# Optimization experiments

Hardware: AMD Instinct MI355X
Metric: run time of the kernel (lower is better)

Reference implementation:

```python
import jax, jax.numpy as jnp
import numpy as np

B, C, N = 16, 3, 4096
K = 20
IN_CH, HID, OUT_CH = 2 * C, 64, 64
EPS = 1e-5
NEG_SLOPE = 0.2


def setup_inputs() -> dict:
    key = jax.random.key(0)
    ks = jax.random.split(key, 4)
    return {
        "x": jax.random.normal(ks[0], (B, C, N), dtype=jnp.float32),
        "W1": jax.random.normal(ks[1], (HID, IN_CH), dtype=jnp.float32) * 0.1,
        "W2": jax.random.normal(ks[2], (HID, HID), dtype=jnp.float32) * 0.1,
        "W3": jax.random.normal(ks[3], (OUT_CH, HID), dtype=jnp.float32) * 0.1,
        "g1": jnp.ones((HID,), jnp.float32),
        "b1": jnp.zeros((HID,), jnp.float32),
        "g2": jnp.ones((OUT_CH,), jnp.float32),
        "b2": jnp.zeros((OUT_CH,), jnp.float32),
    }


def _lrelu(y):
    return jnp.where(y > 0, y, NEG_SLOPE * y)


def _bn(y, gamma, beta):
    # training-mode BatchNorm2d: stats over all axes except channel (last here)
    mu = jnp.mean(y, axis=(0, 1, 2), keepdims=True)
    var = jnp.mean((y - mu) ** 2, axis=(0, 1, 2), keepdims=True)
    return (y - mu) * jax.lax.rsqrt(var + EPS) * gamma + beta


def _graph_feature(x, k):
    # x: [B, C, N] -> DGCNN edge features [B, N, k, 2C]
    xt = jnp.transpose(x, (0, 2, 1))  # [B, N, C]
    sq = jnp.sum(xt * xt, axis=-1)    # [B, N]
    # negative squared pairwise distance (top_k picks nearest, incl. self)
    neg_dist = 2.0 * jnp.einsum('bnc,bmc->bnm', xt, xt) - sq[:, :, None] - sq[:, None, :]
    _, idx = jax.lax.top_k(neg_dist, k)                 # [B, N, k]
    nbr = jax.vmap(lambda xb, ib: xb[ib])(xt, idx)      # [B, N, k, C] gather
    xc = jnp.broadcast_to(xt[:, :, None, :], nbr.shape)
    return jnp.concatenate([nbr - xc, xc], axis=-1)     # [B, N, k, 2C]


def reference(x, W1, W2, W3, g1, b1, g2, b2):
    f = _graph_feature(x, K)                    # [B, N, k, 2C]
    # 1x1 convs over channel axis (last), matching NCHW permute(0,3,2,1)
    y = jnp.einsum('bnkc,oc->bnko', f, W1)
    y = _bn(_lrelu(y), g1, b1)
    y = jnp.einsum('bnkc,oc->bnko', y, W2)
    y = _bn(_lrelu(y), g1, b1)                  # norm1 is reused (shared params)
    y = jnp.einsum('bnkc,oc->bnko', y, W3)
    y = _bn(_lrelu(y), g2, b2)
    y = jnp.max(y, axis=2)                      # max over k neighbors -> [B, N, out]
    return jnp.transpose(y, (0, 2, 1))          # [B, out, N]
```

## Files before the change

### kernel.cpp

```cpp
#include <hip/hip_runtime.h>
#include <math.h>

#define KNN 20
#define CNT_INV (1.0f / 1310720.0f)

typedef short bf16x8 __attribute__((ext_vector_type(8)));
typedef float f32x4  __attribute__((ext_vector_type(4)));

__device__ __forceinline__ short f2bf(float f) {
  unsigned u = __builtin_bit_cast(unsigned, f);
  u += 0x7FFFu + ((u >> 16) & 1u);
  return (short)(u >> 16);
}
__device__ __forceinline__ float lrelu(float y) { return y > 0.f ? y : 0.2f * y; }

__global__ __launch_bounds__(256) void xt4_kernel(const float* __restrict__ x,
                                                  float4* __restrict__ xt4) {
  const int t = blockIdx.x * 256 + threadIdx.x;
  const int b = t >> 12, m = t & 4095;
  const float* xb = x + (size_t)b * 12288;
  const float a = xb[m], c = xb[4096 + m], e = xb[8192 + m];
  xt4[t] = make_float4(a, c, e, a * a + c * c + e * e);
}

__global__ __launch_bounds__(256) void knn_kernel(const float4* __restrict__ xt4,
                                                  int* __restrict__ idx_out,
                                                  const float* __restrict__ W1,
                                                  float* __restrict__ s1buf) {
  __shared__ int hist[512];
  __shared__ int sB[4];
  __shared__ int wcnt[2][4];
  __shared__ int slist[2][64];
  __shared__ int scnt[2];
  __shared__ int eidx[2][KNN];
  __shared__ float redS[2][128], redQ[2][128];
  const int tid = threadIdx.x, lane = tid & 63, wid = tid >> 6;
  const int p0 = blockIdx.x * 2;
  const int b = p0 >> 12, n0 = p0 & 4095;
  const float4* xb4 = xt4 + (size_t)b * 4096;
  const float4 cpa = xb4[n0], cpb = xb4[n0 + 1];

  float w1r[6];
#pragma unroll
  for (int c = 0; c < 6; ++c) w1r[c] = W1[lane * 6 + c];

  float da[16], db[16];
#pragma unroll
  for (int i = 0; i < 16; ++i) {
    const float4 qv = xb4[i * 256 + tid];
    const float dta = fmaf(cpa.x, qv.x, fmaf(cpa.y, qv.y, cpa.z * qv.z));
    const float dtb = fmaf(cpb.x, qv.x, fmaf(cpb.y, qv.y, cpb.z * qv.z));
    da[i] = fmaxf(fmaf(-2.0f, dta, qv.w) + cpa.w, 0.0f);
    db[i] = fmaxf(fmaf(-2.0f, dtb, qv.w) + cpb.w, 0.0f);
  }

  float lo0 = 0.f, R0 = 1.f, lo1 = 0.f, R1 = 1.f;
  int before0 = 0, before1 = 0;
  float Dedge0 = 1e30f, Dedge1 = 1e30f;
  bool done0 = false, done1 = false;
  for (int pass = 0; pass < 6 && !(done0 && done1); ++pass) {
    hist[tid] = 0; hist[256 + tid] = 0;
    __syncthreads();
    const float sc0 = 256.0f / R0, sc1 = 256.0f / R1;
#pragma unroll
    for (int i = 0; i < 16; ++i) {
      if (!done0) {
        const float rel = da[i] - lo0;
        if (rel >= 0.0f && rel < R0) {
          int bin = (int)(rel * sc0); bin = bin > 255 ? 255 : bin;
          atomicAdd(&hist[bin], 1);
        }
      }
      if (!done1) {
        const float rel = db[i] - lo1;
        if (rel >= 0.0f && rel < R1) {
          int bin = (int)(rel * sc1); bin = bin > 255 ? 255 : bin;
          atomicAdd(&hist[256 + bin], 1);
        }
      }
    }
    __syncthreads();
    if (wid < 2) {
      const bool skip = wid ? done1 : done0;
      if (!skip) {
        const int* h = &hist[wid * 256];
        int s0 = h[lane], s1 = h[64 + lane], s2 = h[128 + lane], s3 = h[192 + lane];
#pragma unroll
        for (int off = 1; off < 64; off <<= 1) { const int t = __shfl_up(s0, off); if (lane >= off) s0 += t; }
#pragma unroll
        for (int off = 1; off < 64; off <<= 1) { const int t = __shfl_up(s1, off); if (lane >= off) s1 += t; }
#pragma unroll
        for (int off = 1; off < 64; off <<= 1) { const int t = __shfl_up(s2, off); if (lane >= off) s2 += t; }
#pragma unroll
        for (int off = 1; off < 64; off <<= 1) { const int t = __shfl_up(s3, off); if (lane >= off) s3 += t; }
        s1 += __shfl(s0, 63);
        s2 += __shfl(s1, 63);
        s3 += __shfl(s2, 63);
        const int bef = wid ? before1 : before0;
        s0 += bef; s1 += bef; s2 += bef; s3 += bef;
        int B = 256, cnt = 0;
        unsigned long long m = __ballot(s0 >= 20);
        if (m) { const int l = __ffsll((long long)m) - 1; B = l; cnt = __shfl(s0, l); }
        else if ((m = __ballot(s1 >= 20)) != 0ull) { const int l = __ffsll((long long)m) - 1; B = 64 + l; cnt = __shfl(s1, l); }
        else if ((m = __ballot(s2 >= 20)) != 0ull) { const int l = __ffsll((long long)m) - 1; B = 128 + l; cnt = __shfl(s2, l); }
        else if ((m = __ballot(s3 >= 20)) != 0ull) { const int l = __ffsll((long long)m) - 1; B = 192 + l; cnt = __shfl(s3, l); }
        if (lane == 0) { sB[wid * 2] = B; sB[wid * 2 + 1] = cnt; }
      }
    }
    __syncthreads();
    bool zoom0 = false, zoom1 = false;
    if (!done0) {
      const int B = sB[0], cnt = sB[1];
      if (B == 256) R0 *= 16.0f;
      else {
        const float bw = R0 * (1.0f / 256.0f);
        Dedge0 = lo0 + (float)(B + 1) * bw;
        if (cnt <= 48) done0 = true;
        else { lo0 += (float)B * bw; R0 = bw; zoom0 = true; }
      }
    }
    if (!done1) {
      const int B = sB[2], cnt = sB[3];
      if (B == 256) R1 *= 16.0f;
      else {
        const float bw = R1 * (1.0f / 256.0f);
        Dedge1 = lo1 + (float)(B + 1) * bw;
        if (cnt <= 48) done1 = true;
        else { lo1 += (float)B * bw; R1 = bw; zoom1 = true; }
      }
    }
    if (zoom0) {
      int c = 0;
#pragma unroll
      for (int i = 0; i < 16; ++i) c += (int)__popcll(__ballot(da[i] < lo0));
      if (lane == 0) wcnt[0][wid] = c;
    }
    if (zoom1) {
      int c = 0;
#pragma unroll
      for (int i = 0; i < 16; ++i) c += (int)__popcll(__ballot(db[i] < lo1));
      if (lane == 0) wcnt[1][wid] = c;
    }
    if (zoom0 || zoom1) {
      __syncthreads();
      if (zoom0) before0 = wcnt[0][0] + wcnt[0][1] + wcnt[0][2] + wcnt[0][3];
      if (zoom1) before1 = wcnt[1][0] + wcnt[1][1] + wcnt[1][2] + wcnt[1][3];
    }
  }

  if (tid < 2) scnt[tid] = 0;
  __syncthreads();
  const float Dthr0 = Dedge0 + 4e-3f, Dthr1 = Dedge1 + 4e-3f;
#pragma unroll
  for (int i = 0; i < 16; ++i) {
    if (da[i] < Dthr0) {
      const int pos = atomicAdd(&scnt[0], 1);
      if (pos < 64) slist[0][pos] = i * 256 + tid;
    }
    if (db[i] < Dthr1) {
      const int pos = atomicAdd(&scnt[1], 1);
      if (pos < 64) slist[1][pos] = i * 256 + tid;
    }
  }
  __syncthreads();

  if (wid < 2) {
    const int s = min(scnt[wid], 64);
    const float4 cp = wid ? cpb : cpa;
    int myi = -1; double myd = -1.0e300;
    if (lane < s) {
      myi = slist[wid][lane];
      const float4 av = xb4[myi];
      const double c0 = (double)cp.x, c1 = (double)cp.y, c2 = (double)cp.z;
      const double a0 = (double)av.x, a1 = (double)av.y, a2 = (double)av.z;
      const double dot = c0 * a0 + c1 * a1 + c2 * a2;
      const double sqm = a0 * a0 + a1 * a1 + a2 * a2;
      const double sn  = c0 * c0 + c1 * c1 + c2 * c2;
      myd = (2.0 * dot - sn) - sqm;
    }
    int rank = 0;
    for (int j = 0; j < s; ++j) {
      const double od = __shfl(myd, j);
      const int    oi = __shfl(myi, j);
      if (od > myd || (od == myd && oi < myi)) ++rank;
    }
    if (lane < s && rank < KNN) {
      idx_out[(p0 + wid) * KNN + rank] = myi;
      eidx[wid][rank] = myi;
    }
  }
  __syncthreads();

  const int q = wid >> 1, kb = wid & 1;
  const float4 cp = q ? cpb : cpa;
  float sm = 0.f, sq = 0.f;
#pragma unroll
  for (int t = 0; t < 10; ++t) {
    const int kk = eidx[q][kb * 10 + t];
    const float4 qv = xb4[kk];
    float y = w1r[0] * (qv.x - cp.x) + w1r[1] * (qv.y - cp.y) +
              w1r[2] * (qv.z - cp.z) +
              w1r[3] * cp.x + w1r[4] * cp.y + w1r[5] * cp.z;
    y = lrelu(y);
    sm += y; sq += y * y;
  }
  redS[q][kb * 64 + lane] = sm; redQ[q][kb * 64 + lane] = sq;
  __syncthreads();
  if (tid < 128) {
    const int q2 = tid >> 6, l2 = tid & 63;
    const float s  = redS[q2][l2] + redS[q2][64 + l2];
    const float qq = redQ[q2][l2] + redQ[q2][64 + l2];
    float* bk = s1buf + (size_t)((p0 + q2) & 255) * 128;
    atomicAdd(&bk[l2], s);
    atomicAdd(&bk[64 + l2], qq);
  }
}

template <int STAGE, int MINW>
__global__ __launch_bounds__(256, MINW) void stage_kernel(
    const float4* __restrict__ xt4, const int* __restrict__ nbr,
    const float* __restrict__ W1,
    const float* __restrict__ w2ft, const float* __restrict__ b2f,
    const float* __restrict__ w3ft, const float* __restrict__ b3f,
    float* __restrict__ sumO, float* __restrict__ sqO,
    float* __restrict__ mx, float* __restrict__ mn) {
  __shared__ float pts[4][96];
  __shared__ float W1T[384];
  __shared__ short abuf[4][2048];
  __shared__ float redS[256], redQ[256];

  const int tid = threadIdx.x, wave = tid >> 6, lane = tid & 63;
  const int q = lane >> 4, cc = lane & 15;

  for (int i = tid; i < 384; i += 256) W1T[i] = W1[(i & 63) * 6 + (i >> 6)];
  __syncthreads();

  float w1r[6];
#pragma unroll
  for (int c = 0; c < 6; ++c) w1r[c] = W1T[c * 64 + lane];

  bf16x8 w2f[2][4];
#pragma unroll
  for (int kt = 0; kt < 2; ++kt)
#pragma unroll
    for (int nt = 0; nt < 4; ++nt)
#pragma unroll
      for (int j = 0; j < 8; ++j)
        w2f[kt][nt][j] = f2bf(w2ft[(kt * 32 + q * 8 + j) * 64 + nt * 16 + cc]);
  float bias2v[4];
#pragma unroll
  for (int nt = 0; nt < 4; ++nt) bias2v[nt] = b2f[nt * 16 + cc];

  bf16x8 w3f[2][4];
  float bias3v[4];
  if (STAGE == 3) {
#pragma unroll
    for (int kt = 0; kt < 2; ++kt)
#pragma unroll
      for (int nt = 0; nt < 4; ++nt)
#pragma unroll
        for (int j = 0; j < 8; ++j)
          w3f[kt][nt][j] = f2bf(w3ft[(kt * 32 + q * 8 + j) * 64 + nt * 16 + cc]);
#pragma unroll
    for (int nt = 0; nt < 4; ++nt) bias3v[nt] = b3f[nt * 16 + cc];
  }

  const int kt1 = lane >> 5, q1 = (lane & 31) >> 3, j1 = lane & 7;
  short* ab = abuf[wave];
  const bf16x8* ab8 = (const bf16x8*)ab;
  float* pw = pts[wave];

  float s_s[4] = {0.f, 0.f, 0.f, 0.f}, s_q[4] = {0.f, 0.f, 0.f, 0.f};
  const int wgid = blockIdx.x * 4 + wave;

  for (int it = 0; it < 8; ++it) {
    const int p = wgid + it * 8192;
    const int b = p >> 12, n = p & 4095;
    const float4* xb4 = xt4 + (size_t)b * 4096;
    if (lane < KNN) {
      const int kk = nbr[p * KNN + lane];
      *(float4*)&pw[lane * 4] = xb4[kk];
    } else if (lane == KNN) {
      *(float4*)&pw[80] = xb4[n];
    }
    const float cx0 = pw[80], cx1 = pw[81], cx2 = pw[82];

#pragma unroll
    for (int k = 0; k < KNN; ++k) {
      const float4 pk = *(const float4*)&pw[k * 4];
      const float f0 = pk.x - cx0, f1 = pk.y - cx1, f2 = pk.z - cx2;
      float y = w1r[0] * f0 + w1r[1] * f1 + w1r[2] * f2 +
                w1r[3] * cx0 + w1r[4] * cx1 + w1r[5] * cx2;
      y = lrelu(y);
      ab[(((k >> 4) * 2 + kt1) * 64 + q1 * 16 + (k & 15)) * 8 + j1] = f2bf(y);
    }

    f32x4 acc2[2][4];
#pragma unroll
    for (int mt = 0; mt < 2; ++mt)
#pragma unroll
      for (int nt = 0; nt < 4; ++nt)
        acc2[mt][nt] = f32x4{bias2v[nt], bias2v[nt], bias2v[nt], bias2v[nt]};
#pragma unroll
    for (int kt = 0; kt < 2; ++kt) {
      const bf16x8 a0 = ab8[(0 * 2 + kt) * 64 + lane];
      const bf16x8 a1 = ab8[(1 * 2 + kt) * 64 + lane];
#pragma unroll
      for (int nt = 0; nt < 4; ++nt) {
        acc2[0][nt] = __builtin_amdgcn_mfma_f32_16x16x32_bf16(a0, w2f[kt][nt], acc2[0][nt], 0, 0, 0);
        acc2[1][nt] = __builtin_amdgcn_mfma_f32_16x16x32_bf16(a1, w2f[kt][nt], acc2[1][nt], 0, 0, 0);
      }
    }

    if (STAGE == 2) {
#pragma unroll
      for (int mt = 0; mt < 2; ++mt)
#pragma unroll
        for (int nt = 0; nt < 4; ++nt)
#pragma unroll
          for (int r = 0; r < 4; ++r) {
            if (mt == 1 && q != 0) continue;
            const float y = lrelu(acc2[mt][nt][r]);
            s_s[nt] += y; s_q[nt] += y * y;
          }
    } else {
#pragma unroll
      for (int mt = 0; mt < 2; ++mt)
#pragma unroll
        for (int nt = 0; nt < 4; ++nt) {
          const int kt3 = nt >> 1;
          const int q3 = (nt & 1) * 2 + (cc >> 3);
          const int j3 = cc & 7;
#pragma unroll
          for (int r = 0; r < 4; ++r) {
            if (mt == 1 && q != 0) continue;
            const float y = lrelu(acc2[mt][nt][r]);
            ab[((mt * 2 + kt3) * 64 + q3 * 16 + q * 4 + r) * 8 + j3] = f2bf(y);
          }
        }

      f32x4 acc3[2][4];
#pragma unroll
      for (int mt = 0; mt < 2; ++mt)
#pragma unroll
        for (int nt = 0; nt < 4; ++nt)
          acc3[mt][nt] = f32x4{bias3v[nt], bias3v[nt], bias3v[nt], bias3v[nt]};
#pragma unroll
      for (int kt = 0; kt < 2; ++kt) {
        const bf16x8 a0 = ab8[(0 * 2 + kt) * 64 + lane];
        const bf16x8 a1 = ab8[(1 * 2 + kt) * 64 + lane];
#pragma unroll
        for (int nt = 0; nt < 4; ++nt) {
          acc3[0][nt] = __builtin_amdgcn_mfma_f32_16x16x32_bf16(a0, w3f[kt][nt], acc3[0][nt], 0, 0, 0);
          acc3[1][nt] = __builtin_amdgcn_mfma_f32_16x16x32_bf16(a1, w3f[kt][nt], acc3[1][nt], 0, 0, 0);
        }
      }

      float vmx[4], vmn[4];
#pragma unroll
      for (int nt = 0; nt < 4; ++nt) { vmx[nt] = -INFINITY; vmn[nt] = INFINITY; }
#pragma unroll
      for (int mt = 0; mt < 2; ++mt)
#pragma unroll
        for (int nt = 0; nt < 4; ++nt)
#pragma unroll
          for (int r = 0; r < 4; ++r) {
            if (mt == 1 && q != 0) continue;
            const float y = lrelu(acc3[mt][nt][r]);
            s_s[nt] += y; s_q[nt] += y * y;
            vmx[nt] = fmaxf(vmx[nt], y); vmn[nt] = fminf(vmn[nt], y);
          }
#pragma unroll
      for (int nt = 0; nt < 4; ++nt) {
        vmx[nt] = fmaxf(vmx[nt], __shfl_xor(vmx[nt], 16));
        vmx[nt] = fmaxf(vmx[nt], __shfl_xor(vmx[nt], 32));
        vmn[nt] = fminf(vmn[nt], __shfl_xor(vmn[nt], 16));
        vmn[nt] = fminf(vmn[nt], __shfl_xor(vmn[nt], 32));
      }
      const float omx = q == 0 ? vmx[0] : q == 1 ? vmx[1] : q == 2 ? vmx[2] : vmx[3];
      const float omn = q == 0 ? vmn[0] : q == 1 ? vmn[1] : q == 2 ? vmn[2] : vmn[3];
      mx[(size_t)p * 64 + lane] = omx;
      mn[(size_t)p * 64 + lane] = omn;
    }
  }

#pragma unroll
  for (int nt = 0; nt < 4; ++nt) {
    s_s[nt] += __shfl_xor(s_s[nt], 16); s_s[nt] += __shfl_xor(s_s[nt], 32);
    s_q[nt] += __shfl_xor(s_q[nt], 16); s_q[nt] += __shfl_xor(s_q[nt], 32);
  }
  const float ms = q == 0 ? s_s[0] : q == 1 ? s_s[1] : q == 2 ? s_s[2] : s_s[3];
  const float mq = q == 0 ? s_q[0] : q == 1 ? s_q[1] : q == 2 ? s_q[2] : s_q[3];
  redS[tid] = ms; redQ[tid] = mq;
  __syncthreads();
  if (tid < 64) {
    const float s  = redS[tid] + redS[64 + tid] + redS[128 + tid] + redS[192 + tid];
    const float qq = redQ[tid] + redQ[64 + tid] + redQ[128 + tid] + redQ[192 + tid];
    atomicAdd(&sumO[tid], s);
    atomicAdd(&sqO[tid], qq);
  }
}

__global__ void fold1_kernel(const float* __restrict__ s1buf,
                             const float* __restrict__ g, const float* __restrict__ bt,
                             const float* __restrict__ W,
                             float* __restrict__ WfT, float* __restrict__ bf) {
  __shared__ float s[64], t[64];
  const int o = threadIdx.x;
  float sm = 0.f, qq = 0.f;
  for (int k = 0; k < 256; ++k) { sm += s1buf[k * 128 + o]; qq += s1buf[k * 128 + 64 + o]; }
  const float mu = sm * CNT_INV;
  const float var = qq * CNT_INV - mu * mu;
  const float sc = g[o] / sqrtf(var + 1e-5f);
  s[o] = sc; t[o] = bt[o] - mu * sc;
  __syncthreads();
  float acc = 0.f;
  for (int c = 0; c < 64; ++c) {
    const float w = W[o * 64 + c];
    WfT[c * 64 + o] = w * s[c];
    acc += w * t[c];
  }
  bf[o] = acc;
}

__global__ void fold_kernel(const float* __restrict__ sum, const float* __restrict__ sq,
                            const float* __restrict__ g, const float* __restrict__ bt,
                            const float* __restrict__ W,
                            float* __restrict__ WfT, float* __restrict__ bf) {
  __shared__ float s[64], t[64];
  const int o = threadIdx.x;
  const float mu = sum[o] * CNT_INV;
  const float var = sq[o] * CNT_INV - mu * mu;
  const float sc = g[o] / sqrtf(var + 1e-5f);
  s[o] = sc; t[o] = bt[o] - mu * sc;
  __syncthreads();
  float acc = 0.f;
  for (int c = 0; c < 64; ++c) {
    const float w = W[o * 64 + c];
    WfT[c * 64 + o] = w * s[c];
    acc += w * t[c];
  }
  bf[o] = acc;
}

__global__ void fold3_kernel(const float* __restrict__ sum, const float* __restrict__ sq,
                             const float* __restrict__ g, const float* __restrict__ bt,
                             float* __restrict__ s3, float* __restrict__ t3) {
  const int o = threadIdx.x;
  const float mu = sum[o] * CNT_INV;
  const float var = sq[o] * CNT_INV - mu * mu;
  const float sc = g[o] / sqrtf(var + 1e-5f);
  s3[o] = sc; t3[o] = bt[o] - mu * sc;
}

__global__ __launch_bounds__(256) void final_kernel(
    const float* __restrict__ mx, const float* __restrict__ mn,
    const float* __restrict__ s3, const float* __restrict__ t3,
    float* __restrict__ out) {
  __shared__ float tmx[64][65], tmn[64][65];
  __shared__ float ss[64], tt[64];
  const int tid = threadIdx.x;
  const int P = blockIdx.x * 64;
  const int b = P >> 12, nb = P & 4095;
  if (tid < 64) { ss[tid] = s3[tid]; tt[tid] = t3[tid]; }
#pragma unroll
  for (int r = 0; r < 16; ++r) {
    const int idx = r * 256 + tid;
    const int pl = idx >> 6, ch = idx & 63;
    const size_t src = ((size_t)(P + pl)) * 64 + ch;
    tmx[pl][ch] = mx[src];
    tmn[pl][ch] = mn[src];
  }
  __syncthreads();
  const int nl = tid & 63;
#pragma unroll
  for (int r = 0; r < 16; ++r) {
    const int o = (tid >> 6) + r * 4;
    const float sc = ss[o];
    const float v = sc >= 0.f ? tmx[nl][o] : tmn[nl][o];
    out[(size_t)b * 262144 + (size_t)o * 4096 + nb + nl] = sc * v + tt[o];
  }
}

extern "C" void kernel_launch(void* const* d_in, const int* in_sizes, int n_in,
                              void* d_out, int out_size, void* d_ws, size_t ws_size,
                              hipStream_t stream) {
  const float* x  = (const float*)d_in[0];
  const float* W1 = (const float*)d_in[1];
  const float* W2 = (const float*)d_in[2];
  const float* W3 = (const float*)d_in[3];
  const float* g1 = (const float*)d_in[4];
  const float* b1 = (const float*)d_in[5];
  const float* g2 = (const float*)d_in[6];
  const float* b2 = (const float*)d_in[7];
  float* out = (float*)d_out;

  char* ws = (char*)d_ws;
  float4* xt4 = (float4*)ws;
  int* idx = (int*)(ws + 1048576);
  float* F = (float*)(ws + 6291456);
  float* sum2 = F + 0,   * sq2 = F + 64;
  float* sum3 = F + 128, * sq3 = F + 192;
  float* s1buf = F + 256;
  float* W2fT = F + 33024;
  float* b2f  = F + 37120;
  float* W3fT = F + 37184;
  float* b3f  = F + 41280;
  float* s3   = F + 41344;
  float* t3   = F + 41408;
  float* mx = (float*)(ws + 6457344);
  float* mn = mx + (size_t)16 * 4096 * 64;

  hipMemsetAsync(F, 0, 33024 * sizeof(float), stream);

  xt4_kernel<<<256, 256, 0, stream>>>(x, xt4);
  knn_kernel<<<32768, 256, 0, stream>>>(xt4, idx, W1, s1buf);
  fold1_kernel<<<1, 64, 0, stream>>>(s1buf, g1, b1, W2, W2fT, b2f);
  stage_kernel<2, 3><<<2048, 256, 0, stream>>>(xt4, idx, W1, W2fT, b2f, nullptr,
                                               nullptr, sum2, sq2, nullptr, nullptr);
  fold_kernel<<<1, 64, 0, stream>>>(sum2, sq2, g1, b1, W3, W3fT, b3f);
  stage_kernel<3, 2><<<2048, 256, 0, stream>>>(xt4, idx, W1, W2fT, b2f, W3fT,
                                               b3f, sum3, sq3, mx, mn);
  fold3_kernel<<<1, 64, 0, stream>>>(sum3, sq3, g2, b2, s3, t3);
  final_kernel<<<1024, 256, 0, stream>>>(mx, mn, s3, t3, out);
}
```

Baseline: 560.6 us.

## Process four query points per kNN block and prefetch neighbor gathers in stages

The kNN kernel now handles four query points per 256-thread block instead of two. This halves the grid and reuses each loaded candidate point across four distance computations. Every wave runs its own histogram scan and rank sort, and the layer-1 statistics are summed per wave without the extra shared-memory reduction and barrier. The stage kernels software-prefetch the next iteration's neighbor indices and gathered points into registers, and fold the W1 centre term into one precomputed base. The cost is more register pressure in the kNN kernel (four 16-element distance arrays), which may lower occupancy.

```diff
diff --git a/kernel.cpp b/kernel.cpp
--- a/kernel.cpp
+++ b/kernel.cpp
@@ -27,61 +27,88 @@
                                                   int* __restrict__ idx_out,
                                                   const float* __restrict__ W1,
                                                   float* __restrict__ s1buf) {
-  __shared__ int hist[512];
-  __shared__ int sB[4];
-  __shared__ int wcnt[2][4];
-  __shared__ int slist[2][64];
-  __shared__ int scnt[2];
-  __shared__ int eidx[2][KNN];
-  __shared__ float redS[2][128], redQ[2][128];
+  __shared__ __align__(16) int hist[1024];
+  __shared__ int sB[8];
+  __shared__ int wcnt[4][4];
+  __shared__ int slist[4][64];
+  __shared__ int scnt[4];
+  __shared__ int eidx[4][KNN];
   const int tid = threadIdx.x, lane = tid & 63, wid = tid >> 6;
-  const int p0 = blockIdx.x * 2;
+  const int p0 = blockIdx.x * 4;
   const int b = p0 >> 12, n0 = p0 & 4095;
   const float4* xb4 = xt4 + (size_t)b * 4096;
-  const float4 cpa = xb4[n0], cpb = xb4[n0 + 1];
+  const float4 cp0 = xb4[n0], cp1 = xb4[n0 + 1], cp2 = xb4[n0 + 2], cp3 = xb4[n0 + 3];
 
   float w1r[6];
 #pragma unroll
   for (int c = 0; c < 6; ++c) w1r[c] = W1[lane * 6 + c];
 
-  float da[16], db[16];
+  float d0[16], d1[16], d2[16], d3[16];
 #pragma unroll
   for (int i = 0; i < 16; ++i) {
     const float4 qv = xb4[i * 256 + tid];
-    const float dta = fmaf(cpa.x, qv.x, fmaf(cpa.y, qv.y, cpa.z * qv.z));
-    const float dtb = fmaf(cpb.x, qv.x, fmaf(cpb.y, qv.y, cpb.z * qv.z));
-    da[i] = fmaxf(fmaf(-2.0f, dta, qv.w) + cpa.w, 0.0f);
-    db[i] = fmaxf(fmaf(-2.0f, dtb, qv.w) + cpb.w, 0.0f);
-  }
-
-  float lo0 = 0.f, R0 = 1.f, lo1 = 0.f, R1 = 1.f;
-  int before0 = 0, before1 = 0;
-  float Dedge0 = 1e30f, Dedge1 = 1e30f;
-  bool done0 = false, done1 = false;
-  for (int pass = 0; pass < 6 && !(done0 && done1); ++pass) {
-    hist[tid] = 0; hist[256 + tid] = 0;
+    const float t0 = fmaf(cp0.x, qv.x, fmaf(cp0.y, qv.y, cp0.z * qv.z));
+    const float t1 = fmaf(cp1.x, qv.x, fmaf(cp1.y, qv.y, cp1.z * qv.z));
+    const float t2 = fmaf(cp2.x, qv.x, fmaf(cp2.y, qv.y, cp2.z * qv.z));
+    const float t3 = fmaf(cp3.x, qv.x, fmaf(cp3.y, qv.y, cp3.z * qv.z));
+    d0[i] = fmaxf(fmaf(-2.0f, t0, qv.w) + cp0.w, 0.0f);
+    d1[i] = fmaxf(fmaf(-2.0f, t1, qv.w) + cp1.w, 0.0f);
+    d2[i] = fmaxf(fmaf(-2.0f, t2, qv.w) + cp2.w, 0.0f);
+    d3[i] = fmaxf(fmaf(-2.0f, t3, qv.w) + cp3.w, 0.0f);
+  }
+
+  float lo0 = 0.f, R0 = 1.f, lo1 = 0.f, R1 = 1.f, lo2 = 0.f, R2 = 1.f, lo3 = 0.f, R3 = 1.f;
+  int bef0 = 0, bef1 = 0, bef2 = 0, bef3 = 0;
+  float Dedge0 = 1e30f, Dedge1 = 1e30f, Dedge2 = 1e30f, Dedge3 = 1e30f;
+  bool dn0 = false, dn1 = false, dn2 = false, dn3 = false;
+  for (int pass = 0; pass < 6 && !(dn0 && dn1 && dn2 && dn3); ++pass) {
+    *(int4*)&hist[tid * 4] = int4{0, 0, 0, 0};
     __syncthreads();
     const float sc0 = 256.0f / R0, sc1 = 256.0f / R1;
-#pragma unroll
-    for (int i = 0; i < 16; ++i) {
-      if (!done0) {
-        const float rel = da[i] - lo0;
+    const float sc2 = 256.0f / R2, sc3 = 256.0f / R3;
+    if (!dn0) {
+#pragma unroll
+      for (int i = 0; i < 16; ++i) {
+        const float rel = d0[i] - lo0;
         if (rel >= 0.0f && rel < R0) {
           int bin = (int)(rel * sc0); bin = bin > 255 ? 255 : bin;
           atomicAdd(&hist[bin], 1);
         }
       }
-      if (!done1) {
-        const float rel = db[i] - lo1;
+    }
+    if (!dn1) {
+#pragma unroll
+      for (int i = 0; i < 16; ++i) {
+        const float rel = d1[i] - lo1;
         if (rel >= 0.0f && rel < R1) {
           int bin = (int)(rel * sc1); bin = bin > 255 ? 255 : bin;
           atomicAdd(&hist[256 + bin], 1);
         }
       }
     }
+    if (!dn2) {
+#pragma unroll
+      for (int i = 0; i < 16; ++i) {
+        const float rel = d2[i] - lo2;
+        if (rel >= 0.0f && rel < R2) {
+          int bin = (int)(rel * sc2); bin = bin > 255 ? 255 : bin;
+          atomicAdd(&hist[512 + bin], 1);
+        }
+      }
+    }
+    if (!dn3) {
+#pragma unroll
+      for (int i = 0; i < 16; ++i) {
+        const float rel = d3[i] - lo3;
+        if (rel >= 0.0f && rel < R3) {
+          int bin = (int)(rel * sc3); bin = bin > 255 ? 255 : bin;
+          atomicAdd(&hist[768 + bin], 1);
+        }
+      }
+    }
     __syncthreads();
-    if (wid < 2) {
-      const bool skip = wid ? done1 : done0;
+    {
+      const bool skip = wid == 0 ? dn0 : wid == 1 ? dn1 : wid == 2 ? dn2 : dn3;
       if (!skip) {
         const int* h = &hist[wid * 256];
         int s0 = h[lane], s1 = h[64 + lane], s2 = h[128 + lane], s3 = h[192 + lane];
@@ -96,7 +123,7 @@
         s1 += __shfl(s0, 63);
         s2 += __shfl(s1, 63);
         s3 += __shfl(s2, 63);
-        const int bef = wid ? before1 : before0;
+        const int bef = wid == 0 ? bef0 : wid == 1 ? bef1 : wid == 2 ? bef2 : bef3;
         s0 += bef; s1 += bef; s2 += bef; s3 += bef;
         int B = 256, cnt = 0;
         unsigned long long m = __ballot(s0 >= 20);
@@ -108,65 +135,108 @@
       }
     }
     __syncthreads();
-    bool zoom0 = false, zoom1 = false;
-    if (!done0) {
-      const int B = sB[0], cnt = sB[1];
-      if (B == 256) R0 *= 16.0f;
+    bool zm0 = false, zm1 = false, zm2 = false, zm3 = false;
+    if (!dn0) {
+      const int Bq = sB[0], cq = sB[1];
+      if (Bq == 256) R0 *= 16.0f;
       else {
         const float bw = R0 * (1.0f / 256.0f);
-        Dedge0 = lo0 + (float)(B + 1) * bw;
-        if (cnt <= 48) done0 = true;
-        else { lo0 += (float)B * bw; R0 = bw; zoom0 = true; }
-      }
-    }
-    if (!done1) {
-      const int B = sB[2], cnt = sB[3];
-      if (B == 256) R1 *= 16.0f;
+        Dedge0 = lo0 + (float)(Bq + 1) * bw;
+        if (cq <= 48) dn0 = true;
+        else { lo0 += (float)Bq * bw; R0 = bw; zm0 = true; }
+      }
+    }
+    if (!dn1) {
+      const int Bq = sB[2], cq = sB[3];
+      if (Bq == 256) R1 *= 16.0f;
       else {
         const float bw = R1 * (1.0f / 256.0f);
-        Dedge1 = lo1 + (float)(B + 1) * bw;
-        if (cnt <= 48) done1 = true;
-        else { lo1 += (float)B * bw; R1 = bw; zoom1 = true; }
-      }
-    }
-    if (zoom0) {
+        Dedge1 = lo1 + (float)(Bq + 1) * bw;
+        if (cq <= 48) dn1 = true;
+        else { lo1 += (float)Bq * bw; R1 = bw; zm1 = true; }
+      }
+    }
+    if (!dn2) {
+      const int Bq = sB[4], cq = sB[5];
+      if (Bq == 256) R2 *= 16.0f;
+      else {
+        const float bw = R2 * (1.0f / 256.0f);
+        Dedge2 = lo2 + (float)(Bq + 1) * bw;
+        if (cq <= 48) dn2 = true;
+        else { lo2 += (float)Bq * bw; R2 = bw; zm2 = true; }
+      }
+    }
+    if (!dn3) {
+      const int Bq = sB[6], cq = sB[7];
+      if (Bq == 256) R3 *= 16.0f;
+      else {
+        const float bw = R3 * (1.0f / 256.0f);
+        Dedge3 = lo3 + (float)(Bq + 1) * bw;
+        if (cq <= 48) dn3 = true;
+        else { lo3 += (float)Bq * bw; R3 = bw; zm3 = true; }
+      }
+    }
+    if (zm0) {
       int c = 0;
 #pragma unroll
-      for (int i = 0; i < 16; ++i) c += (int)__popcll(__ballot(da[i] < lo0));
+      for (int i = 0; i < 16; ++i) c += (int)__popcll(__ballot(d0[i] < lo0));
       if (lane == 0) wcnt[0][wid] = c;
     }
-    if (zoom1) {
+    if (zm1) {
       int c = 0;
 #pragma unroll
-      for (int i = 0; i < 16; ++i) c += (int)__popcll(__ballot(db[i] < lo1));
+      for (int i = 0; i < 16; ++i) c += (int)__popcll(__ballot(d1[i] < lo1));
       if (lane == 0) wcnt[1][wid] = c;
     }
-    if (zoom0 || zoom1) {
+    if (zm2) {
+      int c = 0;
+#pragma unroll
+      for (int i = 0; i < 16; ++i) c += (int)__popcll(__ballot(d2[i] < lo2));
+      if (lane == 0) wcnt[2][wid] = c;
+    }
+    if (zm3) {
+      int c = 0;
+#pragma unroll
+      for (int i = 0; i < 16; ++i) c += (int)__popcll(__ballot(d3[i] < lo3));
+      if (lane == 0) wcnt[3][wid] = c;
+    }
+    if (zm0 | zm1 | zm2 | zm3) {
       __syncthreads();
-      if (zoom0) before0 = wcnt[0][0] + wcnt[0][1] + wcnt[0][2] + wcnt[0][3];
-      if (zoom1) before1 = wcnt[1][0] + wcnt[1][1] + wcnt[1][2] + wcnt[1][3];
-    }
-  }
-
-  if (tid < 2) scnt[tid] = 0;
+      if (zm0) bef0 = wcnt[0][0] + wcnt[0][1] + wcnt[0][2] + wcnt[0][3];
+      if (zm1) bef1 = wcnt[1][0] + wcnt[1][1] + wcnt[1][2] + wcnt[1][3];
+      if (zm2) bef2 = wcnt[2][0] + wcnt[2][1] + wcnt[2][2] + wcnt[2][3];
+      if (zm3) bef3 = wcnt[3][0] + wcnt[3][1] + wcnt[3][2] + wcnt[3][3];
+    }
+  }
+
+  if (tid < 4) scnt[tid] = 0;
   __syncthreads();
-  const float Dthr0 = Dedge0 + 4e-3f, Dthr1 = Dedge1 + 4e-3f;
+  const float T0 = Dedge0 + 4e-3f, T1 = Dedge1 + 4e-3f;
+  const float T2 = Dedge2 + 4e-3f, T3 = Dedge3 + 4e-3f;
 #pragma unroll
   for (int i = 0; i < 16; ++i) {
-    if (da[i] < Dthr0) {
+    if (d0[i] < T0) {
       const int pos = atomicAdd(&scnt[0], 1);
       if (pos < 64) slist[0][pos] = i * 256 + tid;
     }
-    if (db[i] < Dthr1) {
+    if (d1[i] < T1) {
       const int pos = atomicAdd(&scnt[1], 1);
       if (pos < 64) slist[1][pos] = i * 256 + tid;
     }
+    if (d2[i] < T2) {
+      const int pos = atomicAdd(&scnt[2], 1);
+      if (pos < 64) slist[2][pos] = i * 256 + tid;
+    }
+    if (d3[i] < T3) {
+      const int pos = atomicAdd(&scnt[3], 1);
+      if (pos < 64) slist[3][pos] = i * 256 + tid;
+    }
   }
   __syncthreads();
 
-  if (wid < 2) {
+  const float4 cp = wid == 0 ? cp0 : wid == 1 ? cp1 : wid == 2 ? cp2 : cp3;
+  {
     const int s = min(scnt[wid], 64);
-    const float4 cp = wid ? cpb : cpa;
     int myi = -1; double myd = -1.0e300;
     if (lane < s) {
       myi = slist[wid][lane];
@@ -189,31 +259,21 @@
       eidx[wid][rank] = myi;
     }
   }
-  __syncthreads();
-
-  const int q = wid >> 1, kb = wid & 1;
-  const float4 cp = q ? cpb : cpa;
+
+  const float base1 = (w1r[3] - w1r[0]) * cp.x + (w1r[4] - w1r[1]) * cp.y +
+                      (w1r[5] - w1r[2]) * cp.z;
   float sm = 0.f, sq = 0.f;
 #pragma unroll
-  for (int t = 0; t < 10; ++t) {
-    const int kk = eidx[q][kb * 10 + t];
+  for (int t = 0; t < KNN; ++t) {
+    const int kk = eidx[wid][t];
     const float4 qv = xb4[kk];
-    float y = w1r[0] * (qv.x - cp.x) + w1r[1] * (qv.y - cp.y) +
-              w1r[2] * (qv.z - cp.z) +
-              w1r[3] * cp.x + w1r[4] * cp.y + w1r[5] * cp.z;
+    float y = fmaf(w1r[0], qv.x, fmaf(w1r[1], qv.y, fmaf(w1r[2], qv.z, base1)));
     y = lrelu(y);
-    sm += y; sq += y * y;
-  }
-  redS[q][kb * 64 + lane] = sm; redQ[q][kb * 64 + lane] = sq;
-  __syncthreads();
-  if (tid < 128) {
-    const int q2 = tid >> 6, l2 = tid & 63;
-    const float s  = redS[q2][l2] + redS[q2][64 + l2];
-    const float qq = redQ[q2][l2] + redQ[q2][64 + l2];
-    float* bk = s1buf + (size_t)((p0 + q2) & 255) * 128;
-    atomicAdd(&bk[l2], s);
-    atomicAdd(&bk[64 + l2], qq);
-  }
+    sm += y; sq = fmaf(y, y, sq);
+  }
+  float* bk = s1buf + (size_t)((p0 + wid) & 255) * 128;
+  atomicAdd(&bk[lane], sm);
+  atomicAdd(&bk[64 + lane], sq);
 }
 
 template <int STAGE, int MINW>
@@ -273,24 +333,37 @@
   float s_s[4] = {0.f, 0.f, 0.f, 0.f}, s_q[4] = {0.f, 0.f, 0.f, 0.f};
   const int wgid = blockIdx.x * 4 + wave;
 
+  const int stepN = 8192 * KNN;
+  const int* nbp = nbr + (size_t)wgid * KNN + lane;
+  const float4* xb0 = xt4 + (size_t)(wgid >> 12) * 4096;
+  const int nn = wgid & 4095;
+  int kkB = 0;
+  float4 g;
+  if (lane < KNN) {
+    const int kkA = nbp[0];
+    g = xb0[kkA];
+    kkB = nbp[stepN];
+  } else if (lane == KNN) {
+    g = xb0[nn];
+  }
+  const int* nbp2 = nbp + 2 * stepN;
+  const float4* xbn = xb0 + 8192;
+
   for (int it = 0; it < 8; ++it) {
     const int p = wgid + it * 8192;
-    const int b = p >> 12, n = p & 4095;
-    const float4* xb4 = xt4 + (size_t)b * 4096;
-    if (lane < KNN) {
-      const int kk = nbr[p * KNN + lane];
-      *(float4*)&pw[lane * 4] = xb4[kk];
-    } else if (lane == KNN) {
-      *(float4*)&pw[80] = xb4[n];
-    }
+    if (lane <= KNN) *(float4*)&pw[lane * 4] = g;
+    float4 gn = g; int kkC = kkB;
+    if (it < 7 && lane <= KNN) gn = (lane < KNN) ? xbn[kkB] : xbn[nn];
+    if (it < 6 && lane < KNN) kkC = nbp2[0];
+
     const float cx0 = pw[80], cx1 = pw[81], cx2 = pw[82];
+    const float base1 = (w1r[3] - w1r[0]) * cx0 + (w1r[4] - w1r[1]) * cx1 +
+                        (w1r[5] - w1r[2]) * cx2;
 
 #pragma unroll
     for (int k = 0; k < KNN; ++k) {
       const float4 pk = *(const float4*)&pw[k * 4];
-      const float f0 = pk.x - cx0, f1 = pk.y - cx1, f2 = pk.z - cx2;
-      float y = w1r[0] * f0 + w1r[1] * f1 + w1r[2] * f2 +
-                w1r[3] * cx0 + w1r[4] * cx1 + w1r[5] * cx2;
+      float y = fmaf(w1r[0], pk.x, fmaf(w1r[1], pk.y, fmaf(w1r[2], pk.z, base1)));
       y = lrelu(y);
       ab[(((k >> 4) * 2 + kt1) * 64 + q1 * 16 + (k & 15)) * 8 + j1] = f2bf(y);
     }
@@ -382,6 +455,8 @@
       mx[(size_t)p * 64 + lane] = omx;
       mn[(size_t)p * 64 + lane] = omn;
     }
+
+    g = gn; kkB = kkC; nbp2 += stepN; xbn += 8192;
   }
 
 #pragma unroll
@@ -514,7 +589,7 @@
   hipMemsetAsync(F, 0, 33024 * sizeof(float), stream);
 
   xt4_kernel<<<256, 256, 0, stream>>>(x, xt4);
-  knn_kernel<<<32768, 256, 0, stream>>>(xt4, idx, W1, s1buf);
+  knn_kernel<<<16384, 256, 0, stream>>>(xt4, idx, W1, s1buf);
   fold1_kernel<<<1, 64, 0, stream>>>(s1buf, g1, b1, W2, W2fT, b2f);
   stage_kernel<2, 3><<<2048, 256, 0, stream>>>(xt4, idx, W1, W2fT, b2f, nullptr,
                                                nullptr, sum2, sq2, nullptr, nullptr);
```

Measured after the change: 533.1 us. 4.9% less time.
